# Kernel optimization log

Measured on AMD Instinct MI355X. Metric: run time of the kernel, lower is better.

Reference implementation:

```python
import jax, jax.numpy as jnp
import numpy as np

B, C_IN, C_OUT, N, K = 8, 64, 128, 2048, 16
EPS = 1e-5  # torch BatchNorm2d default


def setup_inputs() -> dict:
    key = jax.random.key(0)
    ks = jax.random.split(key, 2)
    x = jax.random.normal(ks[0], (B, C_IN, N, 1), dtype=jnp.float32)
    # Conv2d(2*C_IN, C_OUT, 1) kaiming_normal weight, zero bias; 1x1 kernel -> [C_OUT, 2*C_IN]
    W = jax.random.normal(ks[1], (C_OUT, 2 * C_IN), dtype=jnp.float32) * np.float32(np.sqrt(2.0 / (2 * C_IN)))
    b = jnp.zeros((C_OUT,), jnp.float32)
    gamma = jnp.ones((C_OUT,), jnp.float32)   # BN weight filled with 1
    beta = jnp.zeros((C_OUT,), jnp.float32)   # BN bias zeroed
    return {"x": x, "W": W, "b": b, "gamma": gamma, "beta": beta, "k": K}


def reference(x, W, b, gamma, beta, k):
    # x: [B, C, N, 1]
    xs = x[..., 0]                              # [B, C, N]
    feats = jnp.transpose(xs, (0, 2, 1))        # [B, N, C]
    # knn: pairwise_distance = -||xi||^2 + 2 xi.xj - ||xj||^2 (negative sq dist)
    sq = jnp.sum(xs * xs, axis=1)               # [B, N]
    gram = jnp.einsum('bcn,bcm->bnm', xs, xs)   # [B, N, N]
    pd = 2.0 * gram - sq[:, :, None] - sq[:, None, :]
    idx = jax.lax.top_k(pd, k)[1]               # [B, N, k] neighbor indices
    # gather: x_j = neighbor features, x_i = center features broadcast over k
    x_j = jnp.take_along_axis(feats[:, None, :, :], idx[:, :, :, None], axis=2)  # [B, N, k, C]
    x_i = feats[:, :, None, :]                  # [B, N, 1, C]
    e = jnp.concatenate([jnp.broadcast_to(x_i, x_j.shape), x_j - x_i], axis=-1)  # [B, N, k, 2C]
    # 1x1 conv (matmul over channels) + ReLU
    h = jax.nn.relu(jnp.einsum('bnkc,oc->bnko', e, W) + b)  # [B, N, k, O]
    # BatchNorm2d in training mode: batch stats over (B, N, k), biased variance
    mean = jnp.mean(h, axis=(0, 1, 2))
    var = jnp.mean(jnp.square(h - mean), axis=(0, 1, 2))
    h = (h - mean) * jax.lax.rsqrt(var + EPS) * gamma + beta
    # max over neighbors, back to [B, O, N, 1]
    out = jnp.max(h, axis=2)                    # [B, N, O]
    return jnp.transpose(out, (0, 2, 1))[..., None]
```

## Files before the change

### kernel.cpp

```cpp
#include <hip/hip_runtime.h>
#include <math.h>

#define BB 8
#define CIN 64
#define CO 128
#define NPT 2048
#define KK 16
#define EPSV 1e-5f
#define LOSCALE 2048.0f

typedef unsigned int u32;
typedef unsigned long long u64;
typedef _Float16 f16x8 __attribute__((ext_vector_type(8)));
typedef float f32x4 __attribute__((ext_vector_type(4)));

__global__ __launch_bounds__(256) void k_wsplit(
    const float* __restrict__ W, _Float16* __restrict__ wdh,
    _Float16* __restrict__ wdl, _Float16* __restrict__ w2h,
    _Float16* __restrict__ w2l) {
  int i = blockIdx.x * 256 + threadIdx.x;
  int o = i >> 6, c = i & 63;
  float w1 = W[o * 2 * CIN + c];
  float w2 = W[o * 2 * CIN + CIN + c];
  float wd = w1 - w2;
  _Float16 h2 = (_Float16)w2;
  w2h[i] = h2;
  w2l[i] = (_Float16)((w2 - (float)h2) * LOSCALE);
  _Float16 hd = (_Float16)wd;
  wdh[i] = hd;
  wdl[i] = (_Float16)((wd - (float)hd) * LOSCALE);
}

__global__ __launch_bounds__(256) void k_prep_pv(
    const float* __restrict__ x, const float* __restrict__ bias,
    const _Float16* __restrict__ wdh, const _Float16* __restrict__ wdl,
    const _Float16* __restrict__ w2h, const _Float16* __restrict__ w2l,
    float* __restrict__ sq, _Float16* __restrict__ xh,
    _Float16* __restrict__ xl, float* __restrict__ p, float* __restrict__ v) {
  __shared__ float tile[64][65];
  __shared__ float psum[4][64];
  __shared__ _Float16 xhp[64][72];
  __shared__ _Float16 xlp[64][72];
  int bid = blockIdx.x;
  int b = bid >> 5;
  int n0 = (bid & 31) << 6;
  int tid = threadIdx.x;
  int q = tid >> 6, lo = tid & 63;
#pragma unroll
  for (int i = 0; i < 16; ++i) {
    int c = i * 4 + q;
    tile[c][lo] = x[((size_t)(b * CIN + c)) * NPT + n0 + lo];
  }
  __syncthreads();
  float ps = 0.f;
#pragma unroll
  for (int i = 0; i < 16; ++i) {
    float t = tile[q * 16 + i][lo];
    ps += t * t;
  }
  psum[q][lo] = ps;
#pragma unroll
  for (int i = 0; i < 16; ++i) {
    int ni = i * 4 + q;
    float val = tile[lo][ni];
    size_t o = ((size_t)(b * NPT + n0 + ni)) * CIN + lo;
    _Float16 h = (_Float16)val;
    _Float16 l = (_Float16)((val - (float)h) * LOSCALE);
    xh[o] = h;
    xl[o] = l;
    xhp[ni][lo] = h;
    xlp[ni][lo] = l;
  }
  if (q == 0) {
    sq[(size_t)b * NPT + n0 + lo] = psum[0][lo] + psum[1][lo] + psum[2][lo] + psum[3][lo];
  }
  __syncthreads();

  int w = tid >> 6, lane = tid & 63;
  int lr = lane & 15, lg = lane >> 4;
  f16x8 ah0 = *(const f16x8*)&xhp[w * 16 + lr][lg * 8];
  f16x8 ah1 = *(const f16x8*)&xhp[w * 16 + lr][lg * 8 + 32];
  f16x8 al0 = *(const f16x8*)&xlp[w * 16 + lr][lg * 8];
  f16x8 al1 = *(const f16x8*)&xlp[w * 16 + lr][lg * 8 + 32];
  const float kinv = 1.0f / LOSCALE;
#pragma unroll 1
  for (int ot = 0; ot < 8; ++ot) {
    int orow = ot * 16 + lr;
    const f16x8 bdh0 = *(const f16x8*)(wdh + orow * 64 + lg * 8);
    const f16x8 bdh1 = *(const f16x8*)(wdh + orow * 64 + lg * 8 + 32);
    const f16x8 bdl0 = *(const f16x8*)(wdl + orow * 64 + lg * 8);
    const f16x8 bdl1 = *(const f16x8*)(wdl + orow * 64 + lg * 8 + 32);
    const f16x8 b2h0 = *(const f16x8*)(w2h + orow * 64 + lg * 8);
    const f16x8 b2h1 = *(const f16x8*)(w2h + orow * 64 + lg * 8 + 32);
    const f16x8 b2l0 = *(const f16x8*)(w2l + orow * 64 + lg * 8);
    const f16x8 b2l1 = *(const f16x8*)(w2l + orow * 64 + lg * 8 + 32);
    float bo = bias[orow];
    f32x4 pa0 = {0.f, 0.f, 0.f, 0.f}, pa1 = {0.f, 0.f, 0.f, 0.f};
    f32x4 va0 = {0.f, 0.f, 0.f, 0.f}, va1 = {0.f, 0.f, 0.f, 0.f};
    pa1 = __builtin_amdgcn_mfma_f32_16x16x32_f16(ah0, bdl0, pa1, 0, 0, 0);
    pa1 = __builtin_amdgcn_mfma_f32_16x16x32_f16(al0, bdh0, pa1, 0, 0, 0);
    pa1 = __builtin_amdgcn_mfma_f32_16x16x32_f16(ah1, bdl1, pa1, 0, 0, 0);
    pa1 = __builtin_amdgcn_mfma_f32_16x16x32_f16(al1, bdh1, pa1, 0, 0, 0);
    pa0 = __builtin_amdgcn_mfma_f32_16x16x32_f16(ah0, bdh0, pa0, 0, 0, 0);
    pa0 = __builtin_amdgcn_mfma_f32_16x16x32_f16(ah1, bdh1, pa0, 0, 0, 0);
    va1 = __builtin_amdgcn_mfma_f32_16x16x32_f16(ah0, b2l0, va1, 0, 0, 0);
    va1 = __builtin_amdgcn_mfma_f32_16x16x32_f16(al0, b2h0, va1, 0, 0, 0);
    va1 = __builtin_amdgcn_mfma_f32_16x16x32_f16(ah1, b2l1, va1, 0, 0, 0);
    va1 = __builtin_amdgcn_mfma_f32_16x16x32_f16(al1, b2h1, va1, 0, 0, 0);
    va0 = __builtin_amdgcn_mfma_f32_16x16x32_f16(ah0, b2h0, va0, 0, 0, 0);
    va0 = __builtin_amdgcn_mfma_f32_16x16x32_f16(ah1, b2h1, va0, 0, 0, 0);
#pragma unroll
    for (int qq = 0; qq < 4; ++qq) {
      size_t gn = (size_t)(b * NPT + n0 + w * 16 + lg * 4 + qq) * CO + orow;
      p[gn] = fmaf(pa1[qq], kinv, pa0[qq]) + bo;
      v[gn] = fmaf(va1[qq], kinv, va0[qq]);
    }
  }
}

__global__ __launch_bounds__(1024) void k_dist_topk(
    const _Float16* __restrict__ xh, const _Float16* __restrict__ xl,
    const float* __restrict__ sq, float* p_mx,
    const float* __restrict__ v, float* __restrict__ psums,
    float* __restrict__ psqs) {
  __shared__ uint4 tiles[16][2][256];
  __shared__ float submax[16][64];
  __shared__ float2 cand[16][96];
  __shared__ int cnt[16];
  __shared__ float tauf[16];

  int bid = (blockIdx.x & 7) * 128 + (blockIdx.x >> 3);
  int b = bid >> 7;
  int rt = (bid & 127) << 4;
  int tid = threadIdx.x;
  int w = tid >> 6, lane = tid & 63;
  int lr = lane & 15, lg = lane >> 4;
  const _Float16* xhb = xh + (size_t)b * NPT * CIN;
  const _Float16* xlb = xl + (size_t)b * NPT * CIN;
  const float* sqb = sq + (size_t)b * NPT;

  if (tid < 16) cnt[tid] = 0;

  const size_t arow = (size_t)(rt + lr) * CIN + lg * 8;
  f16x8 ah0 = *(const f16x8*)(xhb + arow);
  f16x8 ah1 = *(const f16x8*)(xhb + arow + 32);
  f16x8 al0 = *(const f16x8*)(xlb + arow);
  f16x8 al1 = *(const f16x8*)(xlb + arow + 32);
  float4 sqr = *(const float4*)(sqb + rt + lg * 4);
  float sqrv[4] = {sqr.x, sqr.y, sqr.z, sqr.w};
  float csqs[8];
#pragma unroll
  for (int t = 0; t < 8; ++t) csqs[t] = sqb[(w * 8 + t) * 16 + lr];

  const char* xhB = (const char*)xhb;
  const char* xlB = (const char*)xlb;
  const int su = (lane ^ ((lane >> 3) & 7)) * 16;

#define ISSUE_TILE(T)                                                          \
  {                                                                            \
    const int tb_ = (w * 8 + (T)) * 2048;                                      \
    uint4* buf_ = &tiles[w][(T) & 1][0];                                       \
    __builtin_amdgcn_global_load_lds((const uint4*)(xhB + tb_ + su),           \
                                     buf_, 16, 0, 0);                          \
    __builtin_amdgcn_global_load_lds((const uint4*)(xhB + tb_ + 1024 + su),    \
                                     buf_ + 64, 16, 0, 0);                     \
    __builtin_amdgcn_global_load_lds((const uint4*)(xlB + tb_ + su),           \
                                     buf_ + 128, 16, 0, 0);                    \
    __builtin_amdgcn_global_load_lds((const uint4*)(xlB + tb_ + 1024 + su),    \
                                     buf_ + 192, 16, 0, 0);                    \
  }

  ISSUE_TILE(0)
  ISSUE_TILE(1)

  const int uh0 = lr * 8 + (lg ^ (lr & 7));
  const int uh1 = lr * 8 + ((lg + 4) ^ (lr & 7));
  float vals[32];

#pragma unroll
  for (int t = 0; t < 8; ++t) {
    if (t < 7) { asm volatile("s_waitcnt vmcnt(4)" ::: "memory"); }
    else       { asm volatile("s_waitcnt vmcnt(0)" ::: "memory"); }
    __builtin_amdgcn_sched_barrier(0);
    const uint4* bufr = &tiles[w][t & 1][0];
    f16x8 bh0 = *(const f16x8*)(bufr + uh0);
    f16x8 bh1 = *(const f16x8*)(bufr + uh1);
    f16x8 bl0 = *(const f16x8*)(bufr + 128 + uh0);
    f16x8 bl1 = *(const f16x8*)(bufr + 128 + uh1);
    asm volatile("s_waitcnt lgkmcnt(0)" ::: "memory");
    __builtin_amdgcn_sched_barrier(0);
    if (t == 0) ISSUE_TILE(2)
    if (t == 1) ISSUE_TILE(3)
    if (t == 2) ISSUE_TILE(4)
    if (t == 3) ISSUE_TILE(5)
    if (t == 4) ISSUE_TILE(6)
    if (t == 5) ISSUE_TILE(7)
    f32x4 acc0 = {0.f, 0.f, 0.f, 0.f};
    f32x4 acc1 = {0.f, 0.f, 0.f, 0.f};
    acc1 = __builtin_amdgcn_mfma_f32_16x16x32_f16(ah0, bl0, acc1, 0, 0, 0);
    acc1 = __builtin_amdgcn_mfma_f32_16x16x32_f16(al0, bh0, acc1, 0, 0, 0);
    acc1 = __builtin_amdgcn_mfma_f32_16x16x32_f16(ah1, bl1, acc1, 0, 0, 0);
    acc1 = __builtin_amdgcn_mfma_f32_16x16x32_f16(al1, bh1, acc1, 0, 0, 0);
    acc0 = __builtin_amdgcn_mfma_f32_16x16x32_f16(ah0, bh0, acc0, 0, 0, 0);
    acc0 = __builtin_amdgcn_mfma_f32_16x16x32_f16(ah1, bh1, acc0, 0, 0, 0);
    const float k2 = 2.0f / LOSCALE;
#pragma unroll
    for (int q = 0; q < 4; ++q) {
      vals[t * 4 + q] = fmaf(acc1[q], k2, 2.f * acc0[q]) - (sqrv[q] + csqs[t]);
    }
  }
#undef ISSUE_TILE

  float rmax[4];
#pragma unroll
  for (int q = 0; q < 4; ++q) {
    float m = vals[q];
#pragma unroll
    for (int t = 1; t < 8; ++t) m = fmaxf(m, vals[t * 4 + q]);
    m = fmaxf(m, __shfl_xor(m, 1, 64));
    m = fmaxf(m, __shfl_xor(m, 2, 64));
    rmax[q] = m;
  }
  if ((lr & 3) == 0) {
    int pool = w * 4 + (lr >> 2);
#pragma unroll
    for (int q = 0; q < 4; ++q) submax[lg * 4 + q][pool] = rmax[q];
  }
  __syncthreads();

  {
    u32 ou = __float_as_uint(submax[w][lane]);
    ou = (ou & 0x80000000u) ? ~ou : (ou | 0x80000000u);
    u32 lo = 0u;
#pragma unroll
    for (int s2 = 31; s2 >= 16; --s2) {
      u32 cd = lo | (1u << s2);
      u64 bal = __ballot(ou >= cd);
      if (__popcll(bal) >= KK) lo = cd;
    }
    u32 tb = (lo & 0x80000000u) ? (lo ^ 0x80000000u) : ~lo;
    if (lane == 0) tauf[w] = __uint_as_float(tb);
  }
  __syncthreads();

  {
    float tq[4];
#pragma unroll
    for (int q = 0; q < 4; ++q) tq[q] = tauf[lg * 4 + q];
#pragma unroll
    for (int t = 0; t < 8; ++t) {
#pragma unroll
      for (int q = 0; q < 4; ++q) {
        float vv = vals[t * 4 + q];
        if (vv >= tq[q]) {
          int r = lg * 4 + q;
          int pos = atomicAdd(&cnt[r], 1);
          if (pos < 96) cand[r][pos] = make_float2(vv, __int_as_float((w * 8 + t) * 16 + lr));
        }
      }
    }
  }
  __syncthreads();

  int total = cnt[w];
  if (total > 96) total = 96;
  const float NINF = -__builtin_inff();
  float cv = NINF;
  int ci = 0x7FFFFFFF;
  int n1 = total < 64 ? total : 64;
  if (lane < n1) {
    float2 pr = cand[w][lane];
    cv = pr.x; ci = __float_as_int(pr.y);
  }

#define PSORT(KMAX)                                                        \
  _Pragma("unroll") for (int k = 2; k <= (KMAX); k <<= 1) {                \
    _Pragma("unroll") for (int j = k >> 1; j > 0; j >>= 1) {               \
      float pv = __shfl_xor(cv, j, 64);                                    \
      int pi = __shfl_xor(ci, j, 64);                                      \
      bool up = (lane & k) != 0;                                           \
      bool lw = (lane & j) == 0;                                           \
      bool gt = (cv > pv) || (cv == pv && ci < pi);                        \
      bool keep = (lw != up) ? gt : !gt;                                   \
      cv = keep ? cv : pv;                                                 \
      ci = keep ? ci : pi;                                                 \
    }                                                                      \
  }

  if (total > 32) {
    PSORT(64)
    if (total > 64) {
      if (lane >= 16) {
        int src2 = 48 + lane;
        if (src2 < total) {
          float2 pr = cand[w][src2];
          cv = pr.x; ci = __float_as_int(pr.y);
        } else { cv = NINF; ci = 0x7FFFFFFF; }
      }
      PSORT(64)
    }
  } else {
    PSORT(32)
  }
#undef PSORT

  {
    int jj[16];
#pragma unroll
    for (int k = 0; k < KK; ++k) jj[k] = __shfl(ci, k, 64) & (NPT - 1);
    size_t gn = (size_t)(b * NPT + rt + w);
    const float* vb = v + (size_t)b * NPT * CO;
    float2 p2 = *(const float2*)(p_mx + gn * CO + lane * 2);
    float2 s2 = {0.f, 0.f}, q2 = {0.f, 0.f}, m2 = {-1e30f, -1e30f};
#pragma unroll
    for (int k = 0; k < KK; ++k) {
      float2 v2 = *(const float2*)(vb + (size_t)jj[k] * CO + lane * 2);
      float h0 = fmaxf(p2.x + v2.x, 0.f);
      float h1 = fmaxf(p2.y + v2.y, 0.f);
      s2.x += h0; s2.y += h1;
      q2.x += h0 * h0; q2.y += h1 * h1;
      m2.x = fmaxf(m2.x, h0); m2.y = fmaxf(m2.y, h1);
    }
    *(float2*)(p_mx + gn * CO + lane * 2) = m2;
    float* sp = (float*)tiles;
    *(float2*)(sp + w * 128 + lane * 2) = s2;
    *(float2*)(sp + 2048 + w * 128 + lane * 2) = q2;
  }
  __syncthreads();
  if (tid < CO) {
    float* sp = (float*)tiles;
    float ts = 0.f, tq = 0.f;
#pragma unroll
    for (int i = 0; i < 16; ++i) { ts += sp[i * 128 + tid]; tq += sp[2048 + i * 128 + tid]; }
    int obid = b * 128 + (rt >> 4);
    psums[(size_t)obid * CO + tid] = ts;
    psqs[(size_t)obid * CO + tid] = tq;
  }
}

__global__ __launch_bounds__(64) void k_final(
    const float* __restrict__ psums, const float* __restrict__ psqs,
    const float* __restrict__ gamma, const float* __restrict__ beta,
    float* __restrict__ scale, float* __restrict__ shift) {
  int o = blockIdx.x;
  int t = threadIdx.x;
  float s = 0.f, q = 0.f;
  for (int i = t; i < BB * (NPT / 16); i += 64) {
    s += psums[(size_t)i * CO + o];
    q += psqs[(size_t)i * CO + o];
  }
#pragma unroll
  for (int d = 32; d >= 1; d >>= 1) {
    s += __shfl_down(s, d, 64);
    q += __shfl_down(q, d, 64);
  }
  if (t == 0) {
    const float M = (float)(BB * NPT * KK);
    float mean = s / M;
    float var = q / M - mean * mean;
    float sc = gamma[o] * rsqrtf(var + EPSV);
    scale[o] = sc;
    shift[o] = beta[o] - mean * sc;
  }
}

__global__ __launch_bounds__(256) void k_out_fast(
    const float* __restrict__ mxb, const float* __restrict__ scale,
    const float* __restrict__ shift, float* __restrict__ out) {
  __shared__ float ob[32][132];
  int bid = blockIdx.x;
  int b = bid >> 6;
  int n0 = (bid & 63) << 5;
  int tid = threadIdx.x;
  int o4 = tid & 31, ns = tid >> 5;
  float4 sc = *(const float4*)(scale + o4 * 4);
  float4 sh = *(const float4*)(shift + o4 * 4);
#pragma unroll
  for (int g = 0; g < 4; ++g) {
    int node = g * 8 + ns;
    size_t po = (size_t)(b * NPT + n0 + node) * CO + o4 * 4;
    float4 mx = *(const float4*)(mxb + po);
    float4 r;
    r.x = mx.x * sc.x + sh.x;
    r.y = mx.y * sc.y + sh.y;
    r.z = mx.z * sc.z + sh.z;
    r.w = mx.w * sc.w + sh.w;
    *(float4*)&ob[node][o4 * 4] = r;
  }
  __syncthreads();
  int ni = tid & 31, oh = tid >> 5;
#pragma unroll
  for (int pass = 0; pass < 16; ++pass) {
    int o = pass * 8 + oh;
    out[((size_t)(b * CO + o)) * NPT + n0 + ni] = ob[ni][o];
  }
}

extern "C" void kernel_launch(void* const* d_in, const int* in_sizes, int n_in,
                              void* d_out, int out_size, void* d_ws, size_t ws_size,
                              hipStream_t stream) {
  const float* x = (const float*)d_in[0];
  const float* W = (const float*)d_in[1];
  const float* bias = (const float*)d_in[2];
  const float* gamma = (const float*)d_in[3];
  const float* beta = (const float*)d_in[4];
  float* out = (float*)d_out;

  char* ws = (char*)d_ws;
  size_t off = 0;
  auto alloc = [&](size_t bytes) {
    void* ptr = ws + off;
    off += (bytes + 255) & ~(size_t)255;
    return ptr;
  };
  _Float16* xh = (_Float16*)alloc(sizeof(_Float16) * BB * NPT * CIN);
  _Float16* xl = (_Float16*)alloc(sizeof(_Float16) * BB * NPT * CIN);
  float* sq = (float*)alloc(sizeof(float) * BB * NPT);
  float* p = (float*)alloc(sizeof(float) * BB * NPT * CO);
  float* v = (float*)alloc(sizeof(float) * BB * NPT * CO);
  float* psums = (float*)alloc(sizeof(float) * BB * (NPT / 16) * CO);
  float* psqs = (float*)alloc(sizeof(float) * BB * (NPT / 16) * CO);
  float* scale = (float*)alloc(sizeof(float) * CO);
  float* shift = (float*)alloc(sizeof(float) * CO);
  _Float16* wdh = (_Float16*)alloc(sizeof(_Float16) * CO * CIN);
  _Float16* wdl = (_Float16*)alloc(sizeof(_Float16) * CO * CIN);
  _Float16* w2h = (_Float16*)alloc(sizeof(_Float16) * CO * CIN);
  _Float16* w2l = (_Float16*)alloc(sizeof(_Float16) * CO * CIN);
  (void)ws_size; (void)in_sizes; (void)n_in; (void)out_size;

  hipLaunchKernelGGL(k_wsplit, dim3(32), dim3(256), 0, stream, W, wdh, wdl, w2h, w2l);
  hipLaunchKernelGGL(k_prep_pv, dim3(BB * (NPT / 64)), dim3(256), 0, stream,
                     x, bias, wdh, wdl, w2h, w2l, sq, xh, xl, p, v);
  hipLaunchKernelGGL(k_dist_topk, dim3(BB * (NPT / 16)), dim3(1024), 0, stream,
                     xh, xl, sq, p, v, psums, psqs);
  hipLaunchKernelGGL(k_final, dim3(CO), dim3(64), 0, stream, psums, psqs, gamma, beta, scale, shift);
  hipLaunchKernelGGL(k_out_fast, dim3(BB * (NPT / 32)), dim3(256), 0, stream, p, scale, shift, out);
}
```

Before: 100.8 us.

## Split prep and point-projection into separate kernels with finer-grained parallelism

The fused prep+projection kernel is split into a transpose/split kernel and a separate MFMA projection kernel. The projection kernel launches 4x more blocks, each handling 16 points, with each wave covering two 16-wide output-channel tiles instead of all eight. The aim is more parallelism and shorter per-wave serial MFMA loops. The cost is an extra launch and re-reading xh/xl from global memory instead of LDS.

```diff
diff --git a/kernel.cpp b/kernel.cpp
--- a/kernel.cpp
+++ b/kernel.cpp
@@ -31,16 +31,11 @@
   wdl[i] = (_Float16)((wd - (float)hd) * LOSCALE);
 }
 
-__global__ __launch_bounds__(256) void k_prep_pv(
-    const float* __restrict__ x, const float* __restrict__ bias,
-    const _Float16* __restrict__ wdh, const _Float16* __restrict__ wdl,
-    const _Float16* __restrict__ w2h, const _Float16* __restrict__ w2l,
-    float* __restrict__ sq, _Float16* __restrict__ xh,
-    _Float16* __restrict__ xl, float* __restrict__ p, float* __restrict__ v) {
+__global__ __launch_bounds__(256) void k_prep(
+    const float* __restrict__ x, float* __restrict__ sq,
+    _Float16* __restrict__ xh, _Float16* __restrict__ xl) {
   __shared__ float tile[64][65];
   __shared__ float psum[4][64];
-  __shared__ _Float16 xhp[64][72];
-  __shared__ _Float16 xlp[64][72];
   int bid = blockIdx.x;
   int b = bid >> 5;
   int n0 = (bid & 31) << 6;
@@ -65,27 +60,36 @@
     float val = tile[lo][ni];
     size_t o = ((size_t)(b * NPT + n0 + ni)) * CIN + lo;
     _Float16 h = (_Float16)val;
-    _Float16 l = (_Float16)((val - (float)h) * LOSCALE);
     xh[o] = h;
-    xl[o] = l;
-    xhp[ni][lo] = h;
-    xlp[ni][lo] = l;
-  }
+    xl[o] = (_Float16)((val - (float)h) * LOSCALE);
+  }
+  __syncthreads();
   if (q == 0) {
     sq[(size_t)b * NPT + n0 + lo] = psum[0][lo] + psum[1][lo] + psum[2][lo] + psum[3][lo];
   }
-  __syncthreads();
-
+}
+
+__global__ __launch_bounds__(256) void k_pv(
+    const _Float16* __restrict__ xh, const _Float16* __restrict__ xl,
+    const _Float16* __restrict__ wdh, const _Float16* __restrict__ wdl,
+    const _Float16* __restrict__ w2h, const _Float16* __restrict__ w2l,
+    const float* __restrict__ bias, float* __restrict__ p,
+    float* __restrict__ v) {
+  int bid = (blockIdx.x & 7) * 128 + (blockIdx.x >> 3);
+  int b = bid >> 7;
+  int n0 = (bid & 127) << 4;
+  int tid = threadIdx.x;
   int w = tid >> 6, lane = tid & 63;
   int lr = lane & 15, lg = lane >> 4;
-  f16x8 ah0 = *(const f16x8*)&xhp[w * 16 + lr][lg * 8];
-  f16x8 ah1 = *(const f16x8*)&xhp[w * 16 + lr][lg * 8 + 32];
-  f16x8 al0 = *(const f16x8*)&xlp[w * 16 + lr][lg * 8];
-  f16x8 al1 = *(const f16x8*)&xlp[w * 16 + lr][lg * 8 + 32];
+  const size_t arow = ((size_t)(b * NPT + n0 + lr)) * CIN + lg * 8;
+  f16x8 ah0 = *(const f16x8*)(xh + arow);
+  f16x8 ah1 = *(const f16x8*)(xh + arow + 32);
+  f16x8 al0 = *(const f16x8*)(xl + arow);
+  f16x8 al1 = *(const f16x8*)(xl + arow + 32);
   const float kinv = 1.0f / LOSCALE;
 #pragma unroll 1
-  for (int ot = 0; ot < 8; ++ot) {
-    int orow = ot * 16 + lr;
+  for (int half = 0; half < 2; ++half) {
+    int orow = (w * 2 + half) * 16 + lr;
     const f16x8 bdh0 = *(const f16x8*)(wdh + orow * 64 + lg * 8);
     const f16x8 bdh1 = *(const f16x8*)(wdh + orow * 64 + lg * 8 + 32);
     const f16x8 bdl0 = *(const f16x8*)(wdl + orow * 64 + lg * 8);
@@ -111,7 +115,7 @@
     va0 = __builtin_amdgcn_mfma_f32_16x16x32_f16(ah1, b2h1, va0, 0, 0, 0);
 #pragma unroll
     for (int qq = 0; qq < 4; ++qq) {
-      size_t gn = (size_t)(b * NPT + n0 + w * 16 + lg * 4 + qq) * CO + orow;
+      size_t gn = (size_t)(b * NPT + n0 + lg * 4 + qq) * CO + orow;
       p[gn] = fmaf(pa1[qq], kinv, pa0[qq]) + bo;
       v[gn] = fmaf(va1[qq], kinv, va0[qq]);
     }
@@ -429,8 +433,9 @@
   (void)ws_size; (void)in_sizes; (void)n_in; (void)out_size;
 
   hipLaunchKernelGGL(k_wsplit, dim3(32), dim3(256), 0, stream, W, wdh, wdl, w2h, w2l);
-  hipLaunchKernelGGL(k_prep_pv, dim3(BB * (NPT / 64)), dim3(256), 0, stream,
-                     x, bias, wdh, wdl, w2h, w2l, sq, xh, xl, p, v);
+  hipLaunchKernelGGL(k_prep, dim3(BB * (NPT / 64)), dim3(256), 0, stream, x, sq, xh, xl);
+  hipLaunchKernelGGL(k_pv, dim3(BB * (NPT / 16)), dim3(256), 0, stream,
+                     xh, xl, wdh, wdl, w2h, w2l, bias, p, v);
   hipLaunchKernelGGL(k_dist_topk, dim3(BB * (NPT / 16)), dim3(1024), 0, stream,
                      xh, xl, sq, p, v, psums, psqs);
   hipLaunchKernelGGL(k_final, dim3(CO), dim3(64), 0, stream, psums, psqs, gamma, beta, scale, shift);
```

After: 99.31 us. No clear change (-1.5%).
